# Kernel tuning notes

Measured on AMD Instinct MI355X. Metric: run time of the kernel, lower is better.

Reference implementation:

```python
import jax, jax.numpy as jnp
import numpy as np

TILES = 8           # OpenCV createCLAHE default tileGridSize=(8,8)
CLIP_LIMIT = 1.2    # module init arg


def _clahe(img, clip_limit=CLIP_LIMIT, tiles=TILES):
    """CLAHE on a [C,H,W] float image in [0,1]; H,W divisible by `tiles`."""
    C, H, W = img.shape
    th, tw = H // tiles, W // tiles
    area = th * tw
    clip = max(int(clip_limit * area / 256.0), 1)  # OpenCV clip-limit scaling

    # Quantize to 8-bit bins (matches (img*255).astype(uint8) truncation)
    v = jnp.clip((img * 255.0).astype(jnp.int32), 0, 255)        # [C,H,W]

    # ---- per-tile, per-channel 256-bin histogram via segment_sum ----
    ty = jnp.arange(H) // th
    tx = jnp.arange(W) // tw
    tile = ty[:, None] * tiles + tx[None, :]                      # [H,W]
    seg = (jnp.arange(C)[:, None, None] * (tiles * tiles) + tile[None]) * 256 + v
    hist = jax.ops.segment_sum(
        jnp.ones((C * H * W,), jnp.float32), seg.reshape(-1),
        num_segments=C * tiles * tiles * 256,
    ).reshape(C, tiles, tiles, 256)

    # ---- clip + uniform redistribution of excess ----
    clipped = jnp.minimum(hist, jnp.float32(clip))
    excess = (hist - clipped).sum(-1, keepdims=True)
    clipped = clipped + excess / 256.0

    # ---- CDF -> per-tile LUT ----
    cdf = jnp.cumsum(clipped, axis=-1)
    lut = jnp.clip(jnp.round(cdf * (255.0 / area)), 0.0, 255.0)  # [C,T,T,256]

    # ---- bilinear interpolation between the 4 neighboring tile LUTs ----
    fy = (jnp.arange(H, dtype=jnp.float32) + 0.5) / th - 0.5
    fx = (jnp.arange(W, dtype=jnp.float32) + 0.5) / tw - 0.5
    y0 = jnp.clip(jnp.floor(fy), 0, tiles - 1).astype(jnp.int32)
    x0 = jnp.clip(jnp.floor(fx), 0, tiles - 1).astype(jnp.int32)
    ay = jnp.clip(fy - y0.astype(jnp.float32), 0.0, 1.0)
    ax = jnp.clip(fx - x0.astype(jnp.float32), 0.0, 1.0)
    y1 = jnp.minimum(y0 + 1, tiles - 1)
    x1 = jnp.minimum(x0 + 1, tiles - 1)

    ci = jnp.arange(C)[:, None, None]
    Y0, Y1 = y0[None, :, None], y1[None, :, None]
    X0, X1 = x0[None, None, :], x1[None, None, :]
    g00 = lut[ci, Y0, X0, v]
    g01 = lut[ci, Y0, X1, v]
    g10 = lut[ci, Y1, X0, v]
    g11 = lut[ci, Y1, X1, v]

    wy = ay[None, :, None]
    wx = ax[None, None, :]
    top = g00 * (1.0 - wx) + g01 * wx
    bot = g10 * (1.0 - wx) + g11 * wx
    out = top * (1.0 - wy) + bot * wy
    return (out / 255.0).astype(jnp.float32)


def setup_inputs() -> dict:
    key = jax.random.key(0)
    img = jax.random.uniform(key, (3, 4096, 4096), dtype=jnp.float32)
    return {"img": img}


def reference(img):
    # Deterministic baseline: always apply CLAHE (the p-gated identity branch
    # of the torch module is trivial and excluded for correctness testing).
    return _clahe(img)
```

## Files before the change

kernel.cpp:

```cpp
#include <hip/hip_runtime.h>
#include <stdint.h>

#define TILES 8
#define HH 4096
#define WW 4096
#define CC 3
#define TH 512
#define TW 512
#define AREA (TH * TW)
#define CLIPV 1228u

__global__ __launch_bounds__(256) void clahe_hist_kernel(
    const float* __restrict__ img,
    uint32_t* __restrict__ vpack,
    int store_v,
    uint32_t* __restrict__ hist)
{
    __shared__ uint32_t sh[4 * 264];
    const int tid  = threadIdx.x;
    const int wave = tid >> 6;
    uint32_t* myh  = sh + wave * 264;

    for (int i = tid; i < 4 * 264; i += 256) sh[i] = 0;
    __syncthreads();

    const int bid = blockIdx.x;
    const int sub = bid & 15;
    const int tl  = bid >> 4;
    const int tx  = tl & 7;
    const int ty  = (tl >> 3) & 7;
    const int c   = tl >> 6;

    const size_t base = ((size_t)c * HH + (size_t)(ty * TH + sub * 32)) * WW + (size_t)tx * TW;

#pragma unroll 2
    for (int it = 0; it < 16; ++it) {
        const int i  = it * 256 + tid;
        const int rl = i >> 7;
        const int c4 = i & 127;
        const size_t addr = base + (size_t)rl * WW + (size_t)c4 * 4;
        const float4 p = *(const float4*)(img + addr);

        int v0 = min(max((int)(p.x * 255.0f), 0), 255);
        int v1 = min(max((int)(p.y * 255.0f), 0), 255);
        int v2 = min(max((int)(p.z * 255.0f), 0), 255);
        int v3 = min(max((int)(p.w * 255.0f), 0), 255);

        atomicAdd(&myh[v0], 1u);
        atomicAdd(&myh[v1], 1u);
        atomicAdd(&myh[v2], 1u);
        atomicAdd(&myh[v3], 1u);

        if (store_v) {
            uint32_t pk = (uint32_t)v0 | ((uint32_t)v1 << 8) |
                          ((uint32_t)v2 << 16) | ((uint32_t)v3 << 24);
            vpack[addr >> 2] = pk;
        }
    }
    __syncthreads();

    const uint32_t s = sh[tid] + sh[264 + tid] + sh[528 + tid] + sh[792 + tid];
    atomicAdd(&hist[(size_t)tl * 256 + tid], s);
}

__global__ __launch_bounds__(256) void clahe_lut_kernel(
    const uint32_t* __restrict__ hist,
    float* __restrict__ lut)
{
    __shared__ uint32_t exs[4];
    __shared__ float wsum[4];

    const int tid  = threadIdx.x;
    const int wave = tid >> 6;
    const int lane = tid & 63;
    const int blk  = blockIdx.x;

    const uint32_t h  = hist[(size_t)blk * 256 + tid];
    const uint32_t cl = min(h, CLIPV);
    uint32_t ex = h - cl;

#pragma unroll
    for (int d = 32; d > 0; d >>= 1) ex += __shfl_down(ex, d, 64);
    if (lane == 0) exs[wave] = ex;
    __syncthreads();
    const uint32_t extot = exs[0] + exs[1] + exs[2] + exs[3];

    float x = (float)cl + (float)extot * (1.0f / 256.0f);

#pragma unroll
    for (int d = 1; d < 64; d <<= 1) {
        float t = __shfl_up(x, d, 64);
        if (lane >= d) x += t;
    }
    if (lane == 63) wsum[wave] = x;
    __syncthreads();
    float add = 0.0f;
    for (int w = 0; w < wave; ++w) add += wsum[w];
    const float cdf = x + add;

    float l = rintf(cdf * (255.0f / (float)AREA));
    l = fminf(fmaxf(l, 0.0f), 255.0f);
    lut[(size_t)blk * 256 + tid] = l;
}

__global__ __launch_bounds__(256) void clahe_apply_kernel(
    const float* __restrict__ img,
    const uint32_t* __restrict__ vpack,
    const float* __restrict__ lut,
    float* __restrict__ out,
    int use_v)
{
    __shared__ float rb[TILES * 256];

    const int b = blockIdx.x;
    const int y = b & (HH - 1);
    const int c = b >> 12;

    const float fy = ((float)y + 0.5f) * (1.0f / (float)TH) - 0.5f;
    int y0 = (int)floorf(fy);
    y0 = min(max(y0, 0), TILES - 1);
    const float ay = fminf(fmaxf(fy - (float)y0, 0.0f), 1.0f);
    const int y1 = min(y0 + 1, TILES - 1);

    const float* lr0 = lut + ((size_t)(c * TILES + y0) * TILES) * 256;
    const float* lr1 = lut + ((size_t)(c * TILES + y1) * TILES) * 256;

#pragma unroll
    for (int k = 0; k < 8; ++k) {
        const int i = k * 256 + threadIdx.x;
        const float a = lr0[i];
        const float d = lr1[i];
        rb[i] = a + ay * (d - a);
    }
    __syncthreads();

    const size_t rowbase = ((size_t)c * HH + (size_t)y) * (WW / 4);
    const float4* img4 = (const float4*)img;
    float4* out4 = (float4*)out;

#pragma unroll
    for (int s = 0; s < 4; ++s) {
        const int slot = s * 256 + threadIdx.x;

        uint32_t pv = 0;
        float4 p = make_float4(0.f, 0.f, 0.f, 0.f);
        if (use_v) pv = vpack[rowbase + slot];
        else       p  = img4[rowbase + slot];

        const int xbase = slot * 4;
        const float fx0 = ((float)xbase + 0.5f) * (1.0f / (float)TW) - 0.5f;
        int x0 = (int)floorf(fx0);
        x0 = min(max(x0, 0), TILES - 1);
        const int x1 = min(x0 + 1, TILES - 1);
        const float* r0 = rb + x0 * 256;
        const float* r1 = rb + x1 * 256;
        const float fxr = fx0 - (float)x0;

        float res[4];
#pragma unroll
        for (int k = 0; k < 4; ++k) {
            int v;
            if (use_v) {
                v = (int)((pv >> (8 * k)) & 255u);
            } else {
                const float pk = (k == 0) ? p.x : (k == 1) ? p.y : (k == 2) ? p.z : p.w;
                v = min(max((int)(pk * 255.0f), 0), 255);
            }
            const float ax = fminf(fmaxf(fxr + (float)k * (1.0f / (float)TW), 0.0f), 1.0f);
            const float g0 = r0[v];
            const float g1 = r1[v];
            res[k] = (g0 + ax * (g1 - g0)) * (1.0f / 255.0f);
        }
        out4[rowbase + slot] = make_float4(res[0], res[1], res[2], res[3]);
    }
}

extern "C" void kernel_launch(void* const* d_in, const int* in_sizes, int n_in,
                              void* d_out, int out_size, void* d_ws, size_t ws_size,
                              hipStream_t stream)
{
    const float* img = (const float*)d_in[0];
    float* out = (float*)d_out;

    uint8_t* ws = (uint8_t*)d_ws;
    uint32_t* hist = (uint32_t*)ws;
    float*    lut  = (float*)(ws + 196608);
    uint32_t* vpack = (uint32_t*)(ws + 393216);

    const size_t need_v = 393216 + (size_t)CC * HH * WW;
    const int use_v = (ws_size >= need_v) ? 1 : 0;

    hipMemsetAsync(hist, 0, (size_t)CC * 64 * 256 * sizeof(uint32_t), stream);

    clahe_hist_kernel<<<CC * 64 * 16, 256, 0, stream>>>(img, vpack, use_v, hist);
    clahe_lut_kernel<<<CC * 64, 256, 0, stream>>>(hist, lut);
    clahe_apply_kernel<<<CC * HH, 256, 0, stream>>>(img, vpack, lut, out, use_v);
}
```

Before: 382.5 us.

## Batch histogram loads and process eight rows per apply block

The histogram kernel now issues four float4 loads per thread before the atomics, giving more memory-level parallelism. The apply kernel now gives each block eight consecutive rows, which always share the same tile-row pair. The two LUT tile rows are loaded into registers once per block, and only the vertically blended LUT in shared memory is rebuilt per row. This cuts the grid size and the redundant global LUT reads by a factor of eight, in exchange for an extra barrier per row and fewer blocks to hide latency.

Result: no change. 375.6 us (-1.8%).

```diff
diff --git a/kernel.cpp b/kernel.cpp
--- a/kernel.cpp
+++ b/kernel.cpp
@@ -33,28 +33,35 @@
 
     const size_t base = ((size_t)c * HH + (size_t)(ty * TH + sub * 32)) * WW + (size_t)tx * TW;
 
-#pragma unroll 2
-    for (int it = 0; it < 16; ++it) {
-        const int i  = it * 256 + tid;
-        const int rl = i >> 7;
-        const int c4 = i & 127;
-        const size_t addr = base + (size_t)rl * WW + (size_t)c4 * 4;
-        const float4 p = *(const float4*)(img + addr);
-
-        int v0 = min(max((int)(p.x * 255.0f), 0), 255);
-        int v1 = min(max((int)(p.y * 255.0f), 0), 255);
-        int v2 = min(max((int)(p.z * 255.0f), 0), 255);
-        int v3 = min(max((int)(p.w * 255.0f), 0), 255);
-
-        atomicAdd(&myh[v0], 1u);
-        atomicAdd(&myh[v1], 1u);
-        atomicAdd(&myh[v2], 1u);
-        atomicAdd(&myh[v3], 1u);
-
-        if (store_v) {
-            uint32_t pk = (uint32_t)v0 | ((uint32_t)v1 << 8) |
-                          ((uint32_t)v2 << 16) | ((uint32_t)v3 << 24);
-            vpack[addr >> 2] = pk;
+    for (int it = 0; it < 4; ++it) {
+        const int i0 = it * 1024 + tid;
+        size_t addr[4];
+        float4 p[4];
+#pragma unroll
+        for (int j = 0; j < 4; ++j) {
+            const int s  = i0 + j * 256;
+            const int rl = s >> 7;
+            const int c4 = s & 127;
+            addr[j] = base + (size_t)rl * WW + (size_t)c4 * 4;
+            p[j] = *(const float4*)(img + addr[j]);
+        }
+#pragma unroll
+        for (int j = 0; j < 4; ++j) {
+            int v0 = min(max((int)(p[j].x * 255.0f), 0), 255);
+            int v1 = min(max((int)(p[j].y * 255.0f), 0), 255);
+            int v2 = min(max((int)(p[j].z * 255.0f), 0), 255);
+            int v3 = min(max((int)(p[j].w * 255.0f), 0), 255);
+
+            atomicAdd(&myh[v0], 1u);
+            atomicAdd(&myh[v1], 1u);
+            atomicAdd(&myh[v2], 1u);
+            atomicAdd(&myh[v3], 1u);
+
+            if (store_v) {
+                uint32_t pk = (uint32_t)v0 | ((uint32_t)v1 << 8) |
+                              ((uint32_t)v2 << 16) | ((uint32_t)v3 << 24);
+                vpack[addr[j] >> 2] = pk;
+            }
         }
     }
     __syncthreads();
@@ -113,65 +120,77 @@
     __shared__ float rb[TILES * 256];
 
     const int b = blockIdx.x;
-    const int y = b & (HH - 1);
-    const int c = b >> 12;
-
-    const float fy = ((float)y + 0.5f) * (1.0f / (float)TH) - 0.5f;
-    int y0 = (int)floorf(fy);
+    const int g = b & 511;
+    const int c = b >> 9;
+    const int ybase = g * 8;
+    const int tid = threadIdx.x;
+
+    const float fyb = ((float)ybase + 0.5f) * (1.0f / (float)TH) - 0.5f;
+    int y0 = (int)floorf(fyb);
     y0 = min(max(y0, 0), TILES - 1);
-    const float ay = fminf(fmaxf(fy - (float)y0, 0.0f), 1.0f);
     const int y1 = min(y0 + 1, TILES - 1);
 
     const float* lr0 = lut + ((size_t)(c * TILES + y0) * TILES) * 256;
     const float* lr1 = lut + ((size_t)(c * TILES + y1) * TILES) * 256;
 
+    float a0[8], a1[8];
 #pragma unroll
     for (int k = 0; k < 8; ++k) {
-        const int i = k * 256 + threadIdx.x;
-        const float a = lr0[i];
-        const float d = lr1[i];
-        rb[i] = a + ay * (d - a);
-    }
-    __syncthreads();
-
-    const size_t rowbase = ((size_t)c * HH + (size_t)y) * (WW / 4);
+        a0[k] = lr0[k * 256 + tid];
+        a1[k] = lr1[k * 256 + tid];
+    }
+
     const float4* img4 = (const float4*)img;
     float4* out4 = (float4*)out;
 
-#pragma unroll
-    for (int s = 0; s < 4; ++s) {
-        const int slot = s * 256 + threadIdx.x;
-
-        uint32_t pv = 0;
-        float4 p = make_float4(0.f, 0.f, 0.f, 0.f);
-        if (use_v) pv = vpack[rowbase + slot];
-        else       p  = img4[rowbase + slot];
-
-        const int xbase = slot * 4;
-        const float fx0 = ((float)xbase + 0.5f) * (1.0f / (float)TW) - 0.5f;
-        int x0 = (int)floorf(fx0);
-        x0 = min(max(x0, 0), TILES - 1);
-        const int x1 = min(x0 + 1, TILES - 1);
-        const float* r0 = rb + x0 * 256;
-        const float* r1 = rb + x1 * 256;
-        const float fxr = fx0 - (float)x0;
-
-        float res[4];
-#pragma unroll
-        for (int k = 0; k < 4; ++k) {
-            int v;
-            if (use_v) {
-                v = (int)((pv >> (8 * k)) & 255u);
-            } else {
-                const float pk = (k == 0) ? p.x : (k == 1) ? p.y : (k == 2) ? p.z : p.w;
-                v = min(max((int)(pk * 255.0f), 0), 255);
+    for (int r = 0; r < 8; ++r) {
+        const int y = ybase + r;
+        const float fy = ((float)y + 0.5f) * (1.0f / (float)TH) - 0.5f;
+        const float ay = fminf(fmaxf(fy - (float)y0, 0.0f), 1.0f);
+
+        if (r) __syncthreads();
+#pragma unroll
+        for (int k = 0; k < 8; ++k)
+            rb[k * 256 + tid] = a0[k] + ay * (a1[k] - a0[k]);
+        __syncthreads();
+
+        const size_t rowbase = ((size_t)c * HH + (size_t)y) * (WW / 4);
+
+#pragma unroll
+        for (int s = 0; s < 4; ++s) {
+            const int slot = s * 256 + tid;
+
+            uint32_t pv = 0;
+            float4 p = make_float4(0.f, 0.f, 0.f, 0.f);
+            if (use_v) pv = vpack[rowbase + slot];
+            else       p  = img4[rowbase + slot];
+
+            const int xbase = slot * 4;
+            const float fx0 = ((float)xbase + 0.5f) * (1.0f / (float)TW) - 0.5f;
+            int x0 = (int)floorf(fx0);
+            x0 = min(max(x0, 0), TILES - 1);
+            const int x1 = min(x0 + 1, TILES - 1);
+            const float* r0 = rb + x0 * 256;
+            const float* r1 = rb + x1 * 256;
+            const float fxr = fx0 - (float)x0;
+
+            float res[4];
+#pragma unroll
+            for (int k = 0; k < 4; ++k) {
+                int v;
+                if (use_v) {
+                    v = (int)((pv >> (8 * k)) & 255u);
+                } else {
+                    const float pk = (k == 0) ? p.x : (k == 1) ? p.y : (k == 2) ? p.z : p.w;
+                    v = min(max((int)(pk * 255.0f), 0), 255);
+                }
+                const float ax = fminf(fmaxf(fxr + (float)k * (1.0f / (float)TW), 0.0f), 1.0f);
+                const float g0 = r0[v];
+                const float g1 = r1[v];
+                res[k] = (g0 + ax * (g1 - g0)) * (1.0f / 255.0f);
             }
-            const float ax = fminf(fmaxf(fxr + (float)k * (1.0f / (float)TW), 0.0f), 1.0f);
-            const float g0 = r0[v];
-            const float g1 = r1[v];
-            res[k] = (g0 + ax * (g1 - g0)) * (1.0f / 255.0f);
+            out4[rowbase + slot] = make_float4(res[0], res[1], res[2], res[3]);
         }
-        out4[rowbase + slot] = make_float4(res[0], res[1], res[2], res[3]);
     }
 }
 
@@ -194,5 +213,5 @@
 
     clahe_hist_kernel<<<CC * 64 * 16, 256, 0, stream>>>(img, vpack, use_v, hist);
     clahe_lut_kernel<<<CC * 64, 256, 0, stream>>>(hist, lut);
-    clahe_apply_kernel<<<CC * HH, 256, 0, stream>>>(img, vpack, lut, out, use_v);
-}
+    clahe_apply_kernel<<<CC * 512, 256, 0, stream>>>(img, vpack, lut, out, use_v);
+}
```
